# Performance work log

Measured on AMD Instinct MI355X. Metric: run time of the kernel, lower is better.

Reference implementation:

```python
import jax, jax.numpy as jnp
import numpy as np
from jax import lax

NMS_TH = 0.05
TOPK_P = 1000
NMS_IOU = 0.5
NUMDETS = 100
NMS_ITERS = 15
IM = 2048.0
SIZES = [256, 128, 64, 32, 16]
NUM_CLASS = 80


def _make_boxes(key, n):
    k1, k2, k3, k4 = jax.random.split(key, 4)
    cy = jax.random.uniform(k1, (n,)) * IM
    cx = jax.random.uniform(k2, (n,)) * IM
    h = jax.random.uniform(k3, (n,)) * 300.0 + 16.0
    w = jax.random.uniform(k4, (n,)) * 300.0 + 16.0
    # yxyx boxes
    return jnp.stack([cy - h / 2, cx - w / 2, cy + h / 2, cx + w / 2], axis=1)


def setup_inputs() -> dict:
    key = jax.random.key(0)
    inp = {}
    for s, sz in enumerate(SIZES):
        kc = jax.random.fold_in(key, 2 * s)
        kb = jax.random.fold_in(key, 2 * s + 1)
        n = sz * sz
        inp['cls%d' % s] = jax.random.normal(kc, (1, n, NUM_CLASS), jnp.float32) - 2.0
        inp['reg%d' % s] = _make_boxes(kb, n)[None]
    inp['locations'] = jnp.array([0.0, 0.0, IM - 1.0, IM - 1.0, 1024.0, 1024.0], jnp.float32)
    return inp


def _pairwise_iou(a, b):
    # a: (N,4) yxyx, b: (M,4) yxyx -> (N,M)
    area_a = jnp.clip(a[:, 2] - a[:, 0], 0) * jnp.clip(a[:, 3] - a[:, 1], 0)
    area_b = jnp.clip(b[:, 2] - b[:, 0], 0) * jnp.clip(b[:, 3] - b[:, 1], 0)
    iy1 = jnp.maximum(a[:, None, 0], b[None, :, 0])
    ix1 = jnp.maximum(a[:, None, 1], b[None, :, 1])
    iy2 = jnp.minimum(a[:, None, 2], b[None, :, 2])
    ix2 = jnp.minimum(a[:, None, 3], b[None, :, 3])
    inter = jnp.clip(iy2 - iy1, 0) * jnp.clip(ix2 - ix1, 0)
    union = area_a[:, None] + area_b[None, :] - inter
    return inter / jnp.maximum(union, 1e-9)


def _cluster_nms(boxes, scores, classes, valid, iou_th):
    order = jnp.argsort(-scores)
    b = boxes[order]
    s = scores[order]
    c = classes[order]
    v = valid[order]
    iou = jnp.triu(_pairwise_iou(b, b), k=1)  # (K,K)

    def body(B, _):
        max_a = B.max(axis=0)
        keep_col = (max_a <= iou_th).astype(B.dtype)[:, None]
        return iou * keep_col, None

    B, _ = lax.scan(body, iou, None, length=NMS_ITERS)
    keep = (B.max(axis=0) <= iou_th) & v
    return b, s, c, keep


def _per_level(cls_s, reg_s):
    p = jax.nn.sigmoid(cls_s[0])                 # (N, C)
    ps = p.max(axis=1)                           # (N,)
    pi = p.argmax(axis=1).astype(jnp.int32) + 1  # class index, 0 is background
    m = ps > NMS_TH
    ps_m = jnp.where(m, ps, -1.0)
    k = min(TOPK_P, ps_m.shape[0])
    top_s, top_idx = lax.top_k(ps_m, k)
    return top_s, pi[top_idx], reg_s[0][top_idx], m[top_idx]


def reference(cls0, cls1, cls2, cls3, cls4, reg0, reg1, reg2, reg3, reg4, locations):
    levels = [(cls0, reg0), (cls1, reg1), (cls2, reg2), (cls3, reg3), (cls4, reg4)]
    sc, cl, bx, vd = [], [], [], []
    for cls_s, reg_s in levels:
        s_, c_, b_, v_ = _per_level(cls_s, reg_s)
        sc.append(s_); cl.append(c_); bx.append(b_); vd.append(v_)
    scores = jnp.concatenate(sc)
    classes = jnp.concatenate(cl)
    boxes = jnp.concatenate(bx, axis=0)
    valid = jnp.concatenate(vd)
    scores = jnp.where(valid, scores, 0.0)

    vy1, vx1, vy2, vx2 = locations[0], locations[1], locations[2], locations[3]
    ori_h, ori_w = locations[4], locations[5]
    boxes = jnp.stack([
        jnp.maximum(boxes[:, 0], vy1), jnp.maximum(boxes[:, 1], vx1),
        jnp.minimum(boxes[:, 2], vy2), jnp.minimum(boxes[:, 3], vx2)], axis=1)

    b, s, c, keep = _cluster_nms(boxes, scores, classes, valid, NMS_IOU)
    s = jnp.where(keep, s, 0.0)
    top_s, sel = lax.top_k(s, NUMDETS)
    bbox = b[sel]
    cls_out = c[sel]

    # transfer boxes back to original-image coordinates
    sy = ori_h / jnp.maximum(vy2 - vy1, 1e-6)
    sx = ori_w / jnp.maximum(vx2 - vx1, 1e-6)
    bbox = jnp.stack([
        (bbox[:, 0] - vy1) * sy, (bbox[:, 1] - vx1) * sx,
        (bbox[:, 2] - vy1) * sy, (bbox[:, 3] - vx1) * sx], axis=1)
    return bbox, cls_out, top_s
```

## Files before the change

kernel.cpp:

```cpp
#include <hip/hip_runtime.h>
#include <math.h>


#define NANCH 87296
#define NF 4256
#define CAPD 128
#define NITER 16
#define BCAP 512
#define EC 8192
#define NBLK 341
#define BASE20 0xBD4CCu
#define NB20 9216
#define BPT 9

struct InPtrs {
    const float* cls[5];
    const float* reg[5];
    const float* loc;
};

constexpr size_t SZ_HIST  = 5ull * NB20 * 4;
constexpr size_t OFF_HIST = 0;
constexpr size_t OFF_CNT  = OFF_HIST + SZ_HIST;
constexpr size_t OFF_CTR  = OFF_CNT + (size_t)NF * 4;
constexpr size_t ZERO_SZ  = OFF_CTR + 128;
constexpr size_t OFF_SBITS = ((ZERO_SZ + 255) / 256) * 256;
constexpr size_t OFF_CLSV  = OFF_SBITS + (size_t)NANCH * 4;
constexpr size_t OFF_PAR   = OFF_CLSV + (size_t)NANCH * 4;
constexpr size_t OFF_INVB  = OFF_PAR + 128;
constexpr size_t OFF_INVO  = OFF_INVB + (size_t)NBLK * 4;
constexpr size_t OFF_FINK  = ((OFF_INVO + (size_t)NBLK * 4 + 255) / 256) * 256;
constexpr size_t OFF_BBUF  = OFF_FINK + (size_t)NF * 8;
constexpr size_t OFF_SBOX  = OFF_BBUF + 5ull * BCAP * 8;
constexpr size_t OFF_SSC   = OFF_SBOX + (size_t)NF * 16;
constexpr size_t OFF_SCV   = OFF_SSC + (size_t)NF * 4;
constexpr size_t OFF_SAR   = OFF_SCV + (size_t)NF * 4;
constexpr size_t OFF_NBR   = OFF_SAR + (size_t)NF * 4;

__device__ __forceinline__ void lvl_of(int a, int& lev, int& idx) {
    if (a < 65536)      { lev = 0; idx = a; }
    else if (a < 81920) { lev = 1; idx = a - 65536; }
    else if (a < 86016) { lev = 2; idx = a - 81920; }
    else if (a < 87040) { lev = 3; idx = a - 86016; }
    else                { lev = 4; idx = a - 87040; }
}

__device__ __forceinline__ unsigned int fkey(float f) {
    unsigned int u = __float_as_uint(f);
    return u ^ ((u & 0x80000000u) ? 0xFFFFFFFFu : 0x80000000u);
}
__device__ __forceinline__ float funkey(unsigned int k) {
    return __uint_as_float(k ^ ((k & 0x80000000u) ? 0x80000000u : 0xFFFFFFFFu));
}
__device__ __forceinline__ unsigned int bin20_addr(unsigned int v) {
    unsigned int owner = v / BPT;
    unsigned int i = v - owner * BPT;
    return (i << 10) | owner;
}
__device__ __forceinline__ unsigned int ald(const unsigned int* p) {
    return __hip_atomic_load((unsigned int*)p, __ATOMIC_RELAXED, __HIP_MEMORY_SCOPE_AGENT);
}
__device__ __forceinline__ void ast64(unsigned long long* p, unsigned long long v) {
    __hip_atomic_store(p, v, __ATOMIC_RELAXED, __HIP_MEMORY_SCOPE_AGENT);
}
__device__ __forceinline__ unsigned long long ald64(const unsigned long long* p) {
    return __hip_atomic_load((unsigned long long*)p, __ATOMIC_RELAXED, __HIP_MEMORY_SCOPE_AGENT);
}

__global__ __launch_bounds__(1024) void k1_score(InPtrs P, unsigned int* hist,
        unsigned int* sbits, unsigned int* clsv, unsigned int* invBlk) {
    int t = threadIdx.x;
    int a = blockIdx.x * 256 + (t >> 2);
    int k = t & 3;
    int lev, idx; lvl_of(a, lev, idx);
    const float4* row = (const float4*)(P.cls[lev] + (size_t)idx * 80);
    float4 v[5];
    #pragma unroll
    for (int q = 0; q < 5; ++q) v[q] = row[q * 4 + k];
    float best = -INFINITY; int bi = 0;
    #pragma unroll
    for (int q = 0; q < 5; ++q) {
        int c0 = q * 16 + k * 4;
        if (v[q].x > best) { best = v[q].x; bi = c0 + 0; }
        if (v[q].y > best) { best = v[q].y; bi = c0 + 1; }
        if (v[q].z > best) { best = v[q].z; bi = c0 + 2; }
        if (v[q].w > best) { best = v[q].w; bi = c0 + 3; }
    }
    #pragma unroll
    for (int m = 1; m < 4; m <<= 1) {
        float ob = __shfl_xor(best, m, 64);
        int  obi = __shfl_xor(bi, m, 64);
        if (ob > best || (ob == best && obi < bi)) { best = ob; bi = obi; }
    }
    bool lead = (k == 0);
    unsigned int valid = 0;
    if (lead) {
        float score = 1.0f / (1.0f + expf(-best));
        valid = (score > 0.05f) ? 1u : 0u;
        float psm = valid ? score : -1.0f;
        unsigned int sb = fkey(psm);
        sbits[a] = sb;
        clsv[a] = (unsigned int)(bi + 1) | (valid << 31);
        if (valid) {
            unsigned int bin = (sb >> 12) - BASE20;
            atomicAdd(&hist[(size_t)lev * NB20 + bin20_addr(bin)], 1u);
        }
    }
    __shared__ unsigned int wv[16];
    unsigned long long mv = __ballot(lead && valid);
    int lane = t & 63, w = t >> 6;
    if (lane == 0) wv[w] = (unsigned int)__popcll(mv);
    __syncthreads();
    if (t == 0) {
        unsigned int s = 0;
        #pragma unroll
        for (int i = 0; i < 16; ++i) s += wv[i];
        invBlk[blockIdx.x] = 256u - s;
    }
}

__global__ __launch_bounds__(1024) void k2_scan(const unsigned int* hist,
        const unsigned int* invBlk, unsigned int* params, unsigned int* invOff) {
    int t = threadIdx.x;
    if (blockIdx.x == 5) {
        __shared__ unsigned int sv[512];
        __shared__ unsigned int orig[512];
        if (t < 512) {
            unsigned int v = (t < NBLK) ? invBlk[t] : 0u;
            sv[t] = v; orig[t] = v;
        }
        __syncthreads();
        for (int off = 1; off < 512; off <<= 1) {
            unsigned int add = 0;
            if (t < 512 && t >= off) add = sv[t - off];
            __syncthreads();
            if (t < 512) sv[t] += add;
            __syncthreads();
        }
        if (t < NBLK) {
            int segStart = (t < 256) ? 0 : (t < 320) ? 256 : (t < 336) ? 320
                         : (t < 340) ? 336 : 340;
            invOff[t] = sv[t] - orig[t] - (segStart > 0 ? sv[segStart - 1] : 0u);
        }
        return;
    }
    int lev = blockIdx.x;
    unsigned int K = (lev == 4) ? 256u : 1000u;
    const unsigned int* h = hist + (size_t)lev * NB20;
    __shared__ unsigned int seg[1024];
    __shared__ unsigned int suf[1024];
    unsigned int hc[BPT];
    unsigned int s = 0;
    #pragma unroll
    for (int i = 0; i < BPT; ++i) { hc[i] = h[(i << 10) | t]; s += hc[i]; }
    seg[t] = s;
    suf[t] = s;
    __syncthreads();
    for (int off = 1; off < 1024; off <<= 1) {
        unsigned int v = suf[t];
        unsigned int add = (t + off < 1024) ? suf[t + off] : 0u;
        __syncthreads();
        suf[t] = v + add;
        __syncthreads();
    }
    unsigned int totValid = suf[0];
    if (totValid >= K) {
        unsigned int excl = suf[t] - seg[t];
        if (excl < K && excl + seg[t] >= K) {
            unsigned int cum = excl;
            for (int i = BPT - 1; i >= 0; --i) {
                unsigned int c = hc[i];
                if (cum + c >= K) {
                    params[lev] = (unsigned int)(t * BPT + i);
                    params[8 + lev] = K - cum;
                    params[16 + lev] = 0;
                    break;
                }
                cum += c;
            }
        }
    } else if (t == 0) {
        params[lev] = 0;
        params[8 + lev] = 0;
        params[16 + lev] = K - totValid;
    }
}

__global__ __launch_bounds__(256) void k3_compact(const unsigned int* sbits,
        const unsigned int* clsv, const unsigned int* params,
        const unsigned int* invOff, unsigned long long* finKeys,
        unsigned int* ctrs, unsigned long long* bBuf) {
    int blk = blockIdx.x;
    int t = threadIdx.x;
    int a = blk * 256 + t;
    int lev, idx; lvl_of(a, lev, idx);
    unsigned int sb = sbits[a];
    unsigned int cv = clsv[a];
    unsigned int bin = (sb >> 12) - BASE20;
    unsigned int Bs = params[lev];
    unsigned int rNeg = params[16 + lev];
    unsigned int valid = cv >> 31;
    int lane = t & 63, w = t >> 6;
    unsigned long long lt = (1ull << lane) - 1ull;
    __shared__ unsigned int wInv[4], wFin[4], wB[4];
    __shared__ unsigned int baseFin, baseB;
    unsigned long long mInv = __ballot(valid == 0u);
    if (lane == 0) wInv[w] = (unsigned int)__popcll(mInv);
    __syncthreads();
    unsigned int invRank = invOff[blk] + (unsigned int)__popcll(mInv & lt);
    for (int i = 0; i < w; ++i) invRank += wInv[i];
    bool isFin, isB;
    if (valid) {
        isFin = (bin > Bs);
        isB   = (bin == Bs);
    } else {
        isFin = (rNeg > 0) && (invRank < rNeg);
        isB   = false;
    }
    unsigned long long mFin = __ballot(isFin);
    unsigned long long mB   = __ballot(isB);
    if (lane == 0) { wFin[w] = (unsigned int)__popcll(mFin); wB[w] = (unsigned int)__popcll(mB); }
    __syncthreads();
    if (t == 0) {
        unsigned int tf = wFin[0] + wFin[1] + wFin[2] + wFin[3];
        unsigned int tb = wB[0] + wB[1] + wB[2] + wB[3];
        baseFin = tf ? atomicAdd(&ctrs[0], tf) : 0u;
        baseB   = tb ? atomicAdd(&ctrs[1 + lev], tb) : 0u;
    }
    __syncthreads();
    if (isFin || isB) {
        unsigned int composite = ((unsigned int)lev << 16) | (unsigned int)idx;
        unsigned int inv = (~composite) & 0x7FFFFu;
        unsigned int low = (inv << 13) | (valid << 7) | (cv & 0x7Fu);
        unsigned long long key = ((unsigned long long)sb << 32) | low;
        if (isFin) {
            unsigned int p = baseFin + (unsigned int)__popcll(mFin & lt);
            for (int i = 0; i < w; ++i) p += wFin[i];
            if (p < NF) finKeys[p] = key;
        } else {
            unsigned int p = baseB + (unsigned int)__popcll(mB & lt);
            for (int i = 0; i < w; ++i) p += wB[i];
            if (p < BCAP) ast64(&bBuf[(size_t)lev * BCAP + p], key);
        }
    }
    __shared__ unsigned int isLast;
    __shared__ unsigned long long kb[BCAP];
    __shared__ unsigned int posS;
    __syncthreads();
    if (t == 0) {
        asm volatile("s_waitcnt vmcnt(0)" ::: "memory");
        unsigned int r = __hip_atomic_fetch_add(&ctrs[8], 1u,
                             __ATOMIC_RELAXED, __HIP_MEMORY_SCOPE_AGENT);
        isLast = (r == (unsigned int)(NBLK - 1)) ? 1u : 0u;
    }
    __syncthreads();
    if (!isLast) return;
    unsigned int fc = ald(&ctrs[0]);
    if (fc > NF) fc = NF;
    if (t == 0) posS = fc;
    __syncthreads();
    for (int blev = 0; blev < 5; ++blev) {
        unsigned int bc = ald(&ctrs[1 + blev]);
        int n = (bc > BCAP) ? BCAP : (int)bc;
        int r = (int)params[8 + blev];
        if (r > n) r = n;
        if (r > 0) {
            for (int i = t; i < n; i += 256)
                kb[i] = ald64(&bBuf[(size_t)blev * BCAP + i]);
            __syncthreads();
            for (int i = t; i < n; i += 256) {
                unsigned long long my = kb[i];
                unsigned int c = 0;
                for (int j = 0; j < n; ++j) c += (kb[j] > my) ? 1u : 0u;
                if (c < (unsigned int)r) {
                    unsigned int p = atomicAdd(&posS, 1u);
                    if (p < NF) finKeys[p] = my;
                }
            }
            __syncthreads();
        }
    }
    for (int i = (int)posS + t; i < NF; i += 256)
        finKeys[i] = (unsigned long long)i;
}

__global__ __launch_bounds__(1024) void k5_rank(InPtrs P,
        const unsigned long long* finKeys,
        float4* sBox, float* sScore, unsigned int* sCV, float* sArea) {
    __shared__ __align__(16) unsigned long long keys[NF];
    __shared__ unsigned int rnk[64];
    int t = threadIdx.x;
    {
        const ulonglong2* src = (const ulonglong2*)finKeys;
        ulonglong2* dst = (ulonglong2*)keys;
        for (int i = t; i < NF / 2; i += 1024) dst[i] = src[i];
    }
    if (t < 64) rnk[t] = 0;
    __syncthreads();
    int lf = t & 63;
    int seg = t >> 6;
    int f = blockIdx.x * 64 + lf;
    unsigned long long my = (f < NF) ? keys[f] : 0ull;
    if (f < NF) {
        unsigned int c = 0;
        const ulonglong2* kp = (const ulonglong2*)keys + seg * 133;
        #pragma unroll 4
        for (int i = 0; i < 133; ++i) {
            ulonglong2 v = kp[i];
            c += (v.x > my) ? 1u : 0u;
            c += (v.y > my) ? 1u : 0u;
        }
        atomicAdd(&rnk[lf], c);
    }
    __syncthreads();
    if (seg == 0 && f < NF) {
        unsigned int r = rnk[lf];
        unsigned int sb  = (unsigned int)(my >> 32);
        unsigned int low = (unsigned int)my;
        unsigned int composite = (~(low >> 13)) & 0x7FFFFu;
        int lev = composite >> 16;
        int idx = composite & 0xFFFF;
        float4 b = ((const float4*)P.reg[lev])[idx];
        float vy1 = P.loc[0], vx1 = P.loc[1], vy2 = P.loc[2], vx2 = P.loc[3];
        float y1 = fmaxf(b.x, vy1), x1 = fmaxf(b.y, vx1);
        float y2 = fminf(b.z, vy2), x2 = fminf(b.w, vx2);
        float area = __fmul_rn(fmaxf(y2 - y1, 0.0f), fmaxf(x2 - x1, 0.0f));
        unsigned int valid = (low >> 7) & 1u;
        sBox[r] = make_float4(y1, x1, y2, x2);
        sScore[r] = valid ? funkey(sb) : 0.0f;
        sCV[r] = (low & 0x7Fu) | (valid << 31);
        sArea[r] = area;
    }
}

__global__ __launch_bounds__(256) void k6_adj(const float4* sBox,
        const float* sArea, unsigned int* cnt, unsigned short* nbr) {
    int L = blockIdx.x;
    float fr = sqrtf(8.0f * (float)L + 1.0f);
    int jt = (int)((fr - 1.0f) * 0.5f);
    while ((jt + 1) * (jt + 2) / 2 <= L) jt++;
    while (jt * (jt + 1) / 2 > L) jt--;
    int it = L - jt * (jt + 1) / 2;
    __shared__ float4 cb[64]; __shared__ float ca[64];
    __shared__ float4 rb[64]; __shared__ float ra[64];
    int t = threadIdx.x;
    if (t < 64) {
        int j = jt * 64 + t;
        if (j < NF) { cb[t] = sBox[j]; ca[t] = sArea[j]; }
        int i = it * 64 + t;
        if (i < NF) { rb[t] = sBox[i]; ra[t] = sArea[i]; }
    }
    __syncthreads();
    int lj = t & 63;
    int j = jt * 64 + lj;
    if (j >= NF) return;
    float4 B = cb[lj]; float ab = ca[lj];
    for (int li = (t >> 6); li < 64; li += 4) {
        int i = it * 64 + li;
        if (i >= j) continue;
        float4 A = rb[li]; float aa = ra[li];
        float iy1 = fmaxf(A.x, B.x), ix1 = fmaxf(A.y, B.y);
        float iy2 = fminf(A.z, B.z), ix2 = fminf(A.w, B.w);
        float ih = fmaxf(iy2 - iy1, 0.0f), iw = fmaxf(ix2 - ix1, 0.0f);
        float inter = __fmul_rn(ih, iw);
        float uni = __fsub_rn(__fadd_rn(aa, ab), inter);
        float iou = __fdiv_rn(inter, fmaxf(uni, 1e-9f));
        if (iou > 0.5f) {
            unsigned int p = atomicAdd(&cnt[j], 1u);
            if (p < CAPD) nbr[(size_t)j * CAPD + p] = (unsigned short)i;
        }
    }
}

__global__ __launch_bounds__(1024) void k7_nms(InPtrs P, const float4* sBox,
        const float* sScore, const unsigned int* sCV, const unsigned int* cnt,
        const unsigned short* nbr, float* out) {
    __shared__ unsigned int edges[EC];
    __shared__ __align__(4) unsigned char bufA[NF];
    __shared__ __align__(4) unsigned char bufB[NF];
    __shared__ unsigned int wsum[16];
    __shared__ float ploc[6];
    __shared__ unsigned int chg;
    int t = threadIdx.x;
    int lane = t & 63, wid = t >> 6;
    if (t < 6) ploc[t] = P.loc[t];
    const int CH = 5;
    unsigned int dq[CH];
    unsigned int s = 0;
    #pragma unroll
    for (int q = 0; q < CH; ++q) {
        int j = t * CH + q;
        unsigned int d = 0;
        if (j < NF) { d = cnt[j]; if (d > CAPD) d = CAPD; }
        dq[q] = d; s += d;
    }
    unsigned int sc = s;
    #pragma unroll
    for (int o = 1; o < 64; o <<= 1) {
        unsigned int n = __shfl_up(sc, o, 64);
        if (lane >= o) sc += n;
    }
    if (lane == 63) wsum[wid] = sc;
    if (t < 1064) ((unsigned int*)bufA)[t] = 0x01010101u;
    __syncthreads();
    unsigned int wbase = 0, tot = 0;
    #pragma unroll
    for (int i = 0; i < 16; ++i) {
        unsigned int v = wsum[i];
        if (i < wid) wbase += v;
        tot += v;
    }
    unsigned int E = tot;
    bool useLds = (E <= (unsigned int)EC);
    if (useLds) {
        unsigned int base = wbase + sc - s;
        #pragma unroll
        for (int q = 0; q < CH; ++q) {
            int j = t * CH + q;
            if (j < NF) {
                unsigned int d = dq[q];
                const unsigned short* nl = nbr + (size_t)j * CAPD;
                for (unsigned int e = 0; e < d; ++e)
                    edges[base + e] = ((unsigned int)nl[e] << 16) | (unsigned int)j;
                base += d;
            }
        }
    }
    __syncthreads();
    unsigned char* cur = bufA; unsigned char* nxt = bufB;
    for (int itr = 0; itr < NITER; ++itr) {
        if (t < 1064) ((unsigned int*)nxt)[t] = 0x01010101u;
        __syncthreads();
        if (useLds) {
            for (int e = t; e < (int)E; e += 1024) {
                unsigned int pk = edges[e];
                if (cur[pk >> 16]) nxt[pk & 0xFFFFu] = 0;
            }
        } else {
            for (int j = t; j < NF; j += 1024) {
                unsigned int d = cnt[j]; if (d > CAPD) d = CAPD;
                const unsigned short* nl = nbr + (size_t)j * CAPD;
                unsigned int hit = 0;
                for (unsigned int e = 0; e < d; ++e)
                    hit |= (unsigned int)cur[nl[e]];
                if (hit) nxt[j] = 0;
            }
        }
        __syncthreads();
        if (t < 1064 &&
            ((unsigned int*)nxt)[t] != ((unsigned int*)cur)[t]) chg = 1;
        __syncthreads();
        unsigned int done = (chg == 0u);
        unsigned char* tm = cur; cur = nxt; nxt = tm;
        __syncthreads();
        if (t == 0) chg = 0;
        if (done) break;
    }
    int base = t * CH;
    unsigned char kf[CH];
    unsigned int sum = 0;
    #pragma unroll
    for (int q = 0; q < CH; ++q) {
        int j = base + q;
        unsigned char v = 0;
        if (j < NF) v = cur[j] & (unsigned char)(sCV[j] >> 31);
        kf[q] = v; sum += v;
    }
    unsigned int sc2 = sum;
    #pragma unroll
    for (int o = 1; o < 64; o <<= 1) {
        unsigned int n = __shfl_up(sc2, o, 64);
        if (lane >= o) sc2 += n;
    }
    if (lane == 63) wsum[wid] = sc2;
    __syncthreads();
    unsigned int wbase2 = 0, keptTot = 0;
    #pragma unroll
    for (int i = 0; i < 16; ++i) {
        unsigned int v = wsum[i];
        if (i < wid) wbase2 += v;
        keptTot += v;
    }
    unsigned int run = wbase2 + sc2 - sum;
    float vy1 = ploc[0], vx1 = ploc[1], vy2 = ploc[2], vx2 = ploc[3];
    float sy = ploc[4] / fmaxf(vy2 - vy1, 1e-6f);
    float sx = ploc[5] / fmaxf(vx2 - vx1, 1e-6f);
    #pragma unroll
    for (int q = 0; q < CH; ++q) {
        int j = base + q;
        if (j >= NF) break;
        unsigned int slot = 0xFFFFFFFFu;
        float scv = 0.0f;
        if (kf[q]) {
            if (run < 100u) { slot = run; scv = sScore[j]; }
            run++;
        } else if (keptTot < 100u) {
            unsigned int nk = (unsigned int)j - run;
            unsigned int s2 = keptTot + nk;
            if (s2 < 100u) { slot = s2; scv = 0.0f; }
        }
        if (slot < 100u) {
            float4 b = sBox[j];
            out[slot * 4 + 0] = (b.x - vy1) * sy;
            out[slot * 4 + 1] = (b.y - vx1) * sx;
            out[slot * 4 + 2] = (b.z - vy1) * sy;
            out[slot * 4 + 3] = (b.w - vx1) * sx;
            out[400 + slot] = (float)(sCV[j] & 0x7Fu);
            out[500 + slot] = scv;
        }
    }
}

extern "C" void kernel_launch(void* const* d_in, const int* in_sizes, int n_in,
                              void* d_out, int out_size, void* d_ws, size_t ws_size,
                              hipStream_t stream) {
    (void)n_in; (void)out_size; (void)ws_size;
    InPtrs P;
    bool inter = (in_sizes[1] == 65536 * 4);
    for (int s = 0; s < 5; ++s) {
        P.cls[s] = (const float*)d_in[inter ? 2 * s : s];
        P.reg[s] = (const float*)d_in[inter ? 2 * s + 1 : 5 + s];
    }
    P.loc = (const float*)d_in[10];

    char* w = (char*)d_ws;
    unsigned int* hist   = (unsigned int*)(w + OFF_HIST);
    unsigned int* cnt    = (unsigned int*)(w + OFF_CNT);
    unsigned int* ctrs   = (unsigned int*)(w + OFF_CTR);
    unsigned int* sbits  = (unsigned int*)(w + OFF_SBITS);
    unsigned int* clsv   = (unsigned int*)(w + OFF_CLSV);
    unsigned int* params = (unsigned int*)(w + OFF_PAR);
    unsigned int* invBlk = (unsigned int*)(w + OFF_INVB);
    unsigned int* invOff = (unsigned int*)(w + OFF_INVO);
    unsigned long long* finKeys = (unsigned long long*)(w + OFF_FINK);
    unsigned long long* bBuf    = (unsigned long long*)(w + OFF_BBUF);
    float4* sBox  = (float4*)(w + OFF_SBOX);
    float* sScore = (float*)(w + OFF_SSC);
    unsigned int* sCV = (unsigned int*)(w + OFF_SCV);
    float* sArea  = (float*)(w + OFF_SAR);
    unsigned short* nbr = (unsigned short*)(w + OFF_NBR);

    hipMemsetAsync(d_ws, 0, ZERO_SZ, stream);
    k1_score<<<NBLK, 1024, 0, stream>>>(P, hist, sbits, clsv, invBlk);
    k2_scan<<<6, 1024, 0, stream>>>(hist, invBlk, params, invOff);
    k3_compact<<<NBLK, 256, 0, stream>>>(sbits, clsv, params, invOff, finKeys, ctrs, bBuf);
    k5_rank<<<67, 1024, 0, stream>>>(P, finKeys, sBox, sScore, sCV, sArea);
    k6_adj<<<2278, 256, 0, stream>>>(sBox, sArea, cnt, nbr);
    k7_nms<<<1, 1024, 0, stream>>>(P, sBox, sScore, sCV, cnt, nbr, (float*)d_out);
}
```

Measured before the change: 173.0 us.

## Fuse scan, compact and rank kernels; merge adjacency and NMS via last-block pattern

Reduces the pipeline from six launches to three. Each compact block now recomputes the per-level histogram threshold scan and its own invalid-prefix offset redundantly. The last-arriving block merges the tie buckets, and the final 67 arriving blocks spin-wait on a flag, then do the global rank scatter. The adjacency tiles and the cluster NMS are also fused: the last tile block runs the iterative suppression with 256 threads instead of 1024. This removes launch gaps and kernel boundaries, but adds redundant histogram reads, a spin-wait that depends on co-resident blocks, and a single-block NMS with fewer threads and a wider int neighbor array.

```diff
diff --git a/kernel.cpp b/kernel.cpp
--- a/kernel.cpp
+++ b/kernel.cpp
@@ -12,6 +12,8 @@
 #define BASE20 0xBD4CCu
 #define NB20 9216
 #define BPT 9
+#define NTILE 2278
+#define NRANK 67
 
 struct InPtrs {
     const float* cls[5];
@@ -28,8 +30,7 @@
 constexpr size_t OFF_CLSV  = OFF_SBITS + (size_t)NANCH * 4;
 constexpr size_t OFF_PAR   = OFF_CLSV + (size_t)NANCH * 4;
 constexpr size_t OFF_INVB  = OFF_PAR + 128;
-constexpr size_t OFF_INVO  = OFF_INVB + (size_t)NBLK * 4;
-constexpr size_t OFF_FINK  = ((OFF_INVO + (size_t)NBLK * 4 + 255) / 256) * 256;
+constexpr size_t OFF_FINK  = ((OFF_INVB + (size_t)NBLK * 4 + 255) / 256) * 256;
 constexpr size_t OFF_BBUF  = OFF_FINK + (size_t)NF * 8;
 constexpr size_t OFF_SBOX  = OFF_BBUF + 5ull * BCAP * 8;
 constexpr size_t OFF_SSC   = OFF_SBOX + (size_t)NF * 16;
@@ -59,6 +60,9 @@
 }
 __device__ __forceinline__ unsigned int ald(const unsigned int* p) {
     return __hip_atomic_load((unsigned int*)p, __ATOMIC_RELAXED, __HIP_MEMORY_SCOPE_AGENT);
+}
+__device__ __forceinline__ void ast(unsigned int* p, unsigned int v) {
+    __hip_atomic_store(p, v, __ATOMIC_RELAXED, __HIP_MEMORY_SCOPE_AGENT);
 }
 __device__ __forceinline__ void ast64(unsigned long long* p, unsigned long long v) {
     __hip_atomic_store(p, v, __ATOMIC_RELAXED, __HIP_MEMORY_SCOPE_AGENT);
@@ -119,107 +123,103 @@
     }
 }
 
-__global__ __launch_bounds__(1024) void k2_scan(const unsigned int* hist,
-        const unsigned int* invBlk, unsigned int* params, unsigned int* invOff) {
+__global__ __launch_bounds__(256) void k3_all(InPtrs P, const unsigned int* hist,
+        const unsigned int* sbits, const unsigned int* clsv,
+        const unsigned int* invBlk, unsigned int* params, unsigned int* ctrs,
+        unsigned long long* finKeys, unsigned long long* bBuf,
+        float4* sBox, float* sScore, unsigned int* sCV, float* sArea) {
+    int blk = blockIdx.x;
     int t = threadIdx.x;
-    if (blockIdx.x == 5) {
-        __shared__ unsigned int sv[512];
-        __shared__ unsigned int orig[512];
-        if (t < 512) {
-            unsigned int v = (t < NBLK) ? invBlk[t] : 0u;
-            sv[t] = v; orig[t] = v;
-        }
-        __syncthreads();
-        for (int off = 1; off < 512; off <<= 1) {
-            unsigned int add = 0;
-            if (t < 512 && t >= off) add = sv[t - off];
-            __syncthreads();
-            if (t < 512) sv[t] += add;
-            __syncthreads();
-        }
-        if (t < NBLK) {
-            int segStart = (t < 256) ? 0 : (t < 320) ? 256 : (t < 336) ? 320
-                         : (t < 340) ? 336 : 340;
-            invOff[t] = sv[t] - orig[t] - (segStart > 0 ? sv[segStart - 1] : 0u);
-        }
-        return;
-    }
-    int lev = blockIdx.x;
+    int lane = t & 63, wid = t >> 6;
+
+    int lev, segStart;
+    if (blk < 256)      { lev = 0; segStart = 0; }
+    else if (blk < 320) { lev = 1; segStart = 256; }
+    else if (blk < 336) { lev = 2; segStart = 320; }
+    else if (blk < 340) { lev = 3; segStart = 336; }
+    else                { lev = 4; segStart = 340; }
     unsigned int K = (lev == 4) ? 256u : 1000u;
     const unsigned int* h = hist + (size_t)lev * NB20;
-    __shared__ unsigned int seg[1024];
-    __shared__ unsigned int suf[1024];
-    unsigned int hc[BPT];
-    unsigned int s = 0;
-    #pragma unroll
-    for (int i = 0; i < BPT; ++i) { hc[i] = h[(i << 10) | t]; s += hc[i]; }
-    seg[t] = s;
-    suf[t] = s;
+
+    __shared__ union {
+        struct { unsigned int osum[1024]; } pre;
+        struct { unsigned long long kb[BCAP]; } tl;
+        struct { unsigned long long keys[NF]; unsigned int rnk[64]; } rk;
+    } u;
+    __shared__ unsigned int red[4];
+    __shared__ unsigned int sBs, sR, sRneg;
+    __shared__ unsigned int wInv[4], wFin[4], wB[4];
+    __shared__ unsigned int baseFin, baseB, myRank, posS;
+
+    unsigned int s4[4];
+    #pragma unroll
+    for (int c = 0; c < 4; ++c) {
+        int ow = t + (c << 8);
+        unsigned int s = 0;
+        #pragma unroll
+        for (int i = 0; i < BPT; ++i) s += h[(i << 10) | ow];
+        s4[c] = s; u.pre.osum[ow] = s;
+    }
     __syncthreads();
     for (int off = 1; off < 1024; off <<= 1) {
-        unsigned int v = suf[t];
-        unsigned int add = (t + off < 1024) ? suf[t + off] : 0u;
-        __syncthreads();
-        suf[t] = v + add;
-        __syncthreads();
-    }
-    unsigned int totValid = suf[0];
+        unsigned int v[4], a2[4];
+        #pragma unroll
+        for (int c = 0; c < 4; ++c) {
+            int idx = t + (c << 8);
+            v[c] = u.pre.osum[idx];
+            a2[c] = (idx + off < 1024) ? u.pre.osum[idx + off] : 0u;
+        }
+        __syncthreads();
+        #pragma unroll
+        for (int c = 0; c < 4; ++c) { int idx = t + (c << 8); u.pre.osum[idx] = v[c] + a2[c]; }
+        __syncthreads();
+    }
+    unsigned int totValid = u.pre.osum[0];
     if (totValid >= K) {
-        unsigned int excl = suf[t] - seg[t];
-        if (excl < K && excl + seg[t] >= K) {
-            unsigned int cum = excl;
-            for (int i = BPT - 1; i >= 0; --i) {
-                unsigned int c = hc[i];
-                if (cum + c >= K) {
-                    params[lev] = (unsigned int)(t * BPT + i);
-                    params[8 + lev] = K - cum;
-                    params[16 + lev] = 0;
-                    break;
+        #pragma unroll
+        for (int c = 0; c < 4; ++c) {
+            int ow = t + (c << 8);
+            unsigned int osuf = u.pre.osum[ow];
+            unsigned int excl = osuf - s4[c];
+            if (excl < K && osuf >= K) {
+                unsigned int cum = excl;
+                for (int i = BPT - 1; i >= 0; --i) {
+                    unsigned int cc = h[(i << 10) | ow];
+                    if (cum + cc >= K) { sBs = (unsigned int)(ow * BPT + i);
+                                         sR = K - cum; sRneg = 0; break; }
+                    cum += cc;
                 }
-                cum += c;
             }
         }
-    } else if (t == 0) {
-        params[lev] = 0;
-        params[8 + lev] = 0;
-        params[16 + lev] = K - totValid;
-    }
-}
-
-__global__ __launch_bounds__(256) void k3_compact(const unsigned int* sbits,
-        const unsigned int* clsv, const unsigned int* params,
-        const unsigned int* invOff, unsigned long long* finKeys,
-        unsigned int* ctrs, unsigned long long* bBuf) {
-    int blk = blockIdx.x;
-    int t = threadIdx.x;
+    } else if (t == 0) { sBs = 0; sR = 0; sRneg = K - totValid; }
+    unsigned int lsum = 0;
+    for (int i = segStart + t; i < blk; i += 256) lsum += invBlk[i];
+    #pragma unroll
+    for (int m = 1; m < 64; m <<= 1) lsum += __shfl_xor(lsum, m, 64);
+    if (lane == 0) red[wid] = lsum;
+    __syncthreads();
+    unsigned int invOffBlk = red[0] + red[1] + red[2] + red[3];
+    unsigned int Bs = sBs, rNeg = sRneg;
+    if (blk == segStart && t == 0) ast(&params[8 + lev], sR);
+
     int a = blk * 256 + t;
-    int lev, idx; lvl_of(a, lev, idx);
     unsigned int sb = sbits[a];
     unsigned int cv = clsv[a];
     unsigned int bin = (sb >> 12) - BASE20;
-    unsigned int Bs = params[lev];
-    unsigned int rNeg = params[16 + lev];
     unsigned int valid = cv >> 31;
-    int lane = t & 63, w = t >> 6;
     unsigned long long lt = (1ull << lane) - 1ull;
-    __shared__ unsigned int wInv[4], wFin[4], wB[4];
-    __shared__ unsigned int baseFin, baseB;
     unsigned long long mInv = __ballot(valid == 0u);
-    if (lane == 0) wInv[w] = (unsigned int)__popcll(mInv);
-    __syncthreads();
-    unsigned int invRank = invOff[blk] + (unsigned int)__popcll(mInv & lt);
-    for (int i = 0; i < w; ++i) invRank += wInv[i];
+    if (lane == 0) wInv[wid] = (unsigned int)__popcll(mInv);
+    __syncthreads();
+    unsigned int invRank = invOffBlk + (unsigned int)__popcll(mInv & lt);
+    for (int i = 0; i < wid; ++i) invRank += wInv[i];
     bool isFin, isB;
-    if (valid) {
-        isFin = (bin > Bs);
-        isB   = (bin == Bs);
-    } else {
-        isFin = (rNeg > 0) && (invRank < rNeg);
-        isB   = false;
-    }
+    if (valid) { isFin = (bin > Bs); isB = (bin == Bs); }
+    else       { isFin = (rNeg > 0) && (invRank < rNeg); isB = false; }
     unsigned long long mFin = __ballot(isFin);
     unsigned long long mB   = __ballot(isB);
-    if (lane == 0) { wFin[w] = (unsigned int)__popcll(mFin); wB[w] = (unsigned int)__popcll(mB); }
+    if (lane == 0) { wFin[wid] = (unsigned int)__popcll(mFin);
+                     wB[wid]   = (unsigned int)__popcll(mB); }
     __syncthreads();
     if (t == 0) {
         unsigned int tf = wFin[0] + wFin[1] + wFin[2] + wFin[3];
@@ -229,169 +229,179 @@
     }
     __syncthreads();
     if (isFin || isB) {
-        unsigned int composite = ((unsigned int)lev << 16) | (unsigned int)idx;
+        int lidx = a - segStart * 256;
+        unsigned int composite = ((unsigned int)lev << 16) | (unsigned int)lidx;
         unsigned int inv = (~composite) & 0x7FFFFu;
         unsigned int low = (inv << 13) | (valid << 7) | (cv & 0x7Fu);
         unsigned long long key = ((unsigned long long)sb << 32) | low;
         if (isFin) {
             unsigned int p = baseFin + (unsigned int)__popcll(mFin & lt);
-            for (int i = 0; i < w; ++i) p += wFin[i];
-            if (p < NF) finKeys[p] = key;
+            for (int i = 0; i < wid; ++i) p += wFin[i];
+            if (p < NF) ast64(&finKeys[p], key);
         } else {
             unsigned int p = baseB + (unsigned int)__popcll(mB & lt);
-            for (int i = 0; i < w; ++i) p += wB[i];
+            for (int i = 0; i < wid; ++i) p += wB[i];
             if (p < BCAP) ast64(&bBuf[(size_t)lev * BCAP + p], key);
         }
     }
-    __shared__ unsigned int isLast;
-    __shared__ unsigned long long kb[BCAP];
-    __shared__ unsigned int posS;
+
     __syncthreads();
     if (t == 0) {
         asm volatile("s_waitcnt vmcnt(0)" ::: "memory");
-        unsigned int r = __hip_atomic_fetch_add(&ctrs[8], 1u,
-                             __ATOMIC_RELAXED, __HIP_MEMORY_SCOPE_AGENT);
-        isLast = (r == (unsigned int)(NBLK - 1)) ? 1u : 0u;
-    }
-    __syncthreads();
-    if (!isLast) return;
-    unsigned int fc = ald(&ctrs[0]);
-    if (fc > NF) fc = NF;
-    if (t == 0) posS = fc;
-    __syncthreads();
-    for (int blev = 0; blev < 5; ++blev) {
-        unsigned int bc = ald(&ctrs[1 + blev]);
-        int n = (bc > BCAP) ? BCAP : (int)bc;
-        int r = (int)params[8 + blev];
-        if (r > n) r = n;
-        if (r > 0) {
-            for (int i = t; i < n; i += 256)
-                kb[i] = ald64(&bBuf[(size_t)blev * BCAP + i]);
-            __syncthreads();
-            for (int i = t; i < n; i += 256) {
-                unsigned long long my = kb[i];
-                unsigned int c = 0;
-                for (int j = 0; j < n; ++j) c += (kb[j] > my) ? 1u : 0u;
-                if (c < (unsigned int)r) {
-                    unsigned int p = atomicAdd(&posS, 1u);
-                    if (p < NF) finKeys[p] = my;
+        myRank = __hip_atomic_fetch_add(&ctrs[8], 1u,
+                     __ATOMIC_RELAXED, __HIP_MEMORY_SCOPE_AGENT);
+    }
+    __syncthreads();
+    unsigned int rk_ = myRank;
+    if (rk_ < (unsigned int)(NBLK - 1 - NRANK)) return;
+
+    if (rk_ == (unsigned int)(NBLK - 1)) {
+        unsigned int fc = ald(&ctrs[0]);
+        if (fc > NF) fc = NF;
+        if (t == 0) posS = fc;
+        __syncthreads();
+        for (int blev = 0; blev < 5; ++blev) {
+            unsigned int bc = ald(&ctrs[1 + blev]);
+            int n = (bc > BCAP) ? BCAP : (int)bc;
+            int r = (int)ald(&params[8 + blev]);
+            if (r > n) r = n;
+            if (r > 0) {
+                for (int i = t; i < n; i += 256)
+                    u.tl.kb[i] = ald64(&bBuf[(size_t)blev * BCAP + i]);
+                __syncthreads();
+                for (int i = t; i < n; i += 256) {
+                    unsigned long long my = u.tl.kb[i];
+                    unsigned int c = 0;
+                    for (int j = 0; j < n; ++j) c += (u.tl.kb[j] > my) ? 1u : 0u;
+                    if (c < (unsigned int)r) {
+                        unsigned int p = atomicAdd(&posS, 1u);
+                        if (p < NF) ast64(&finKeys[p], my);
+                    }
                 }
+                __syncthreads();
             }
-            __syncthreads();
-        }
-    }
-    for (int i = (int)posS + t; i < NF; i += 256)
-        finKeys[i] = (unsigned long long)i;
-}
-
-__global__ __launch_bounds__(1024) void k5_rank(InPtrs P,
-        const unsigned long long* finKeys,
-        float4* sBox, float* sScore, unsigned int* sCV, float* sArea) {
-    __shared__ __align__(16) unsigned long long keys[NF];
-    __shared__ unsigned int rnk[64];
-    int t = threadIdx.x;
-    {
-        const ulonglong2* src = (const ulonglong2*)finKeys;
-        ulonglong2* dst = (ulonglong2*)keys;
-        for (int i = t; i < NF / 2; i += 1024) dst[i] = src[i];
-    }
-    if (t < 64) rnk[t] = 0;
+        }
+        __syncthreads();
+        for (int i = (int)posS + t; i < NF; i += 256)
+            ast64(&finKeys[i], (unsigned long long)i);
+        __syncthreads();
+        if (t == 0) {
+            asm volatile("s_waitcnt vmcnt(0)" ::: "memory");
+            ast(&ctrs[10], 1u);
+        }
+        return;
+    }
+
+    if (t == 0) {
+        int g = 0;
+        while (ald(&ctrs[10]) == 0u && g < 200000) { __builtin_amdgcn_s_sleep(8); ++g; }
+    }
+    __syncthreads();
+    int rb = (int)rk_ - (NBLK - 1 - NRANK);
+    for (int i = t; i < NF; i += 256) u.rk.keys[i] = ald64(&finKeys[i]);
+    if (t < 64) u.rk.rnk[t] = 0;
     __syncthreads();
     int lf = t & 63;
     int seg = t >> 6;
-    int f = blockIdx.x * 64 + lf;
-    unsigned long long my = (f < NF) ? keys[f] : 0ull;
+    int f = rb * 64 + lf;
+    unsigned long long my = (f < NF) ? u.rk.keys[f] : 0ull;
     if (f < NF) {
         unsigned int c = 0;
-        const ulonglong2* kp = (const ulonglong2*)keys + seg * 133;
-        #pragma unroll 4
-        for (int i = 0; i < 133; ++i) {
-            ulonglong2 v = kp[i];
-            c += (v.x > my) ? 1u : 0u;
-            c += (v.y > my) ? 1u : 0u;
-        }
-        atomicAdd(&rnk[lf], c);
+        const unsigned long long* kp = u.rk.keys + seg * 1064;
+        #pragma unroll 8
+        for (int i = 0; i < 1064; ++i) c += (kp[i] > my) ? 1u : 0u;
+        atomicAdd(&u.rk.rnk[lf], c);
     }
     __syncthreads();
     if (seg == 0 && f < NF) {
-        unsigned int r = rnk[lf];
-        unsigned int sb  = (unsigned int)(my >> 32);
+        unsigned int r = u.rk.rnk[lf];
+        unsigned int sbv = (unsigned int)(my >> 32);
         unsigned int low = (unsigned int)my;
         unsigned int composite = (~(low >> 13)) & 0x7FFFFu;
-        int lev = composite >> 16;
+        int lev2 = composite >> 16;
         int idx = composite & 0xFFFF;
-        float4 b = ((const float4*)P.reg[lev])[idx];
+        float4 b = ((const float4*)P.reg[lev2])[idx];
         float vy1 = P.loc[0], vx1 = P.loc[1], vy2 = P.loc[2], vx2 = P.loc[3];
         float y1 = fmaxf(b.x, vy1), x1 = fmaxf(b.y, vx1);
         float y2 = fminf(b.z, vy2), x2 = fminf(b.w, vx2);
         float area = __fmul_rn(fmaxf(y2 - y1, 0.0f), fmaxf(x2 - x1, 0.0f));
-        unsigned int valid = (low >> 7) & 1u;
+        unsigned int valid2 = (low >> 7) & 1u;
         sBox[r] = make_float4(y1, x1, y2, x2);
-        sScore[r] = valid ? funkey(sb) : 0.0f;
-        sCV[r] = (low & 0x7Fu) | (valid << 31);
+        sScore[r] = valid2 ? funkey(sbv) : 0.0f;
+        sCV[r] = (low & 0x7Fu) | (valid2 << 31);
         sArea[r] = area;
     }
 }
 
-__global__ __launch_bounds__(256) void k6_adj(const float4* sBox,
-        const float* sArea, unsigned int* cnt, unsigned short* nbr) {
-    int L = blockIdx.x;
-    float fr = sqrtf(8.0f * (float)L + 1.0f);
-    int jt = (int)((fr - 1.0f) * 0.5f);
-    while ((jt + 1) * (jt + 2) / 2 <= L) jt++;
-    while (jt * (jt + 1) / 2 > L) jt--;
-    int it = L - jt * (jt + 1) / 2;
+__global__ __launch_bounds__(256) void k6_nms(InPtrs P, const float4* sBox,
+        const float* sArea, const float* sScore, const unsigned int* sCV,
+        unsigned int* cnt, unsigned int* nbr, unsigned int* ctrs,
+        float* __restrict__ out) {
     __shared__ float4 cb[64]; __shared__ float ca[64];
-    __shared__ float4 rb[64]; __shared__ float ra[64];
-    int t = threadIdx.x;
-    if (t < 64) {
-        int j = jt * 64 + t;
-        if (j < NF) { cb[t] = sBox[j]; ca[t] = sArea[j]; }
-        int i = it * 64 + t;
-        if (i < NF) { rb[t] = sBox[i]; ra[t] = sArea[i]; }
-    }
-    __syncthreads();
-    int lj = t & 63;
-    int j = jt * 64 + lj;
-    if (j >= NF) return;
-    float4 B = cb[lj]; float ab = ca[lj];
-    for (int li = (t >> 6); li < 64; li += 4) {
-        int i = it * 64 + li;
-        if (i >= j) continue;
-        float4 A = rb[li]; float aa = ra[li];
-        float iy1 = fmaxf(A.x, B.x), ix1 = fmaxf(A.y, B.y);
-        float iy2 = fminf(A.z, B.z), ix2 = fminf(A.w, B.w);
-        float ih = fmaxf(iy2 - iy1, 0.0f), iw = fmaxf(ix2 - ix1, 0.0f);
-        float inter = __fmul_rn(ih, iw);
-        float uni = __fsub_rn(__fadd_rn(aa, ab), inter);
-        float iou = __fdiv_rn(inter, fmaxf(uni, 1e-9f));
-        if (iou > 0.5f) {
-            unsigned int p = atomicAdd(&cnt[j], 1u);
-            if (p < CAPD) nbr[(size_t)j * CAPD + p] = (unsigned short)i;
-        }
-    }
-}
-
-__global__ __launch_bounds__(1024) void k7_nms(InPtrs P, const float4* sBox,
-        const float* sScore, const unsigned int* sCV, const unsigned int* cnt,
-        const unsigned short* nbr, float* out) {
+    __shared__ float4 rbx[64]; __shared__ float ra[64];
     __shared__ unsigned int edges[EC];
     __shared__ __align__(4) unsigned char bufA[NF];
     __shared__ __align__(4) unsigned char bufB[NF];
-    __shared__ unsigned int wsum[16];
+    __shared__ unsigned int wsum[4];
     __shared__ float ploc[6];
-    __shared__ unsigned int chg;
+    __shared__ unsigned int chg, rk2;
     int t = threadIdx.x;
     int lane = t & 63, wid = t >> 6;
+
+    {
+        int L = blockIdx.x;
+        float fr = sqrtf(8.0f * (float)L + 1.0f);
+        int jt = (int)((fr - 1.0f) * 0.5f);
+        while ((jt + 1) * (jt + 2) / 2 <= L) jt++;
+        while (jt * (jt + 1) / 2 > L) jt--;
+        int it = L - jt * (jt + 1) / 2;
+        if (t < 64) {
+            int j = jt * 64 + t;
+            if (j < NF) { cb[t] = sBox[j]; ca[t] = sArea[j]; }
+            int i = it * 64 + t;
+            if (i < NF) { rbx[t] = sBox[i]; ra[t] = sArea[i]; }
+        }
+        __syncthreads();
+        int lj = t & 63;
+        int j = jt * 64 + lj;
+        if (j < NF) {
+            float4 B = cb[lj]; float ab = ca[lj];
+            for (int li = (t >> 6); li < 64; li += 4) {
+                int i = it * 64 + li;
+                if (i >= j) continue;
+                float4 A = rbx[li]; float aa = ra[li];
+                float iy1 = fmaxf(A.x, B.x), ix1 = fmaxf(A.y, B.y);
+                float iy2 = fminf(A.z, B.z), ix2 = fminf(A.w, B.w);
+                float ih = fmaxf(iy2 - iy1, 0.0f), iw = fmaxf(ix2 - ix1, 0.0f);
+                float inter = __fmul_rn(ih, iw);
+                float uni = __fsub_rn(__fadd_rn(aa, ab), inter);
+                float iou = __fdiv_rn(inter, fmaxf(uni, 1e-9f));
+                if (iou > 0.5f) {
+                    unsigned int p = atomicAdd(&cnt[j], 1u);
+                    if (p < CAPD) ast(&nbr[(size_t)j * CAPD + p], (unsigned int)i);
+                }
+            }
+        }
+    }
+    __syncthreads();
+    if (t == 0) {
+        asm volatile("s_waitcnt vmcnt(0)" ::: "memory");
+        rk2 = __hip_atomic_fetch_add(&ctrs[9], 1u,
+                  __ATOMIC_RELAXED, __HIP_MEMORY_SCOPE_AGENT);
+    }
+    __syncthreads();
+    if (rk2 != (unsigned int)(NTILE - 1)) return;
+
+    const int CH = 17;
     if (t < 6) ploc[t] = P.loc[t];
-    const int CH = 5;
+    if (t == 0) chg = 0;
     unsigned int dq[CH];
     unsigned int s = 0;
     #pragma unroll
     for (int q = 0; q < CH; ++q) {
         int j = t * CH + q;
         unsigned int d = 0;
-        if (j < NF) { d = cnt[j]; if (d > CAPD) d = CAPD; }
+        if (j < NF) { d = ald(&cnt[j]); if (d > CAPD) d = CAPD; }
         dq[q] = d; s += d;
     }
     unsigned int sc = s;
@@ -401,11 +411,11 @@
         if (lane >= o) sc += n;
     }
     if (lane == 63) wsum[wid] = sc;
-    if (t < 1064) ((unsigned int*)bufA)[t] = 0x01010101u;
+    for (int i = t; i < 1064; i += 256) ((unsigned int*)bufA)[i] = 0x01010101u;
     __syncthreads();
     unsigned int wbase = 0, tot = 0;
     #pragma unroll
-    for (int i = 0; i < 16; ++i) {
+    for (int i = 0; i < 4; ++i) {
         unsigned int v = wsum[i];
         if (i < wid) wbase += v;
         tot += v;
@@ -419,9 +429,9 @@
             int j = t * CH + q;
             if (j < NF) {
                 unsigned int d = dq[q];
-                const unsigned short* nl = nbr + (size_t)j * CAPD;
+                const unsigned int* nl = nbr + (size_t)j * CAPD;
                 for (unsigned int e = 0; e < d; ++e)
-                    edges[base + e] = ((unsigned int)nl[e] << 16) | (unsigned int)j;
+                    edges[base + e] = (ald(&nl[e]) << 16) | (unsigned int)j;
                 base += d;
             }
         }
@@ -429,26 +439,26 @@
     __syncthreads();
     unsigned char* cur = bufA; unsigned char* nxt = bufB;
     for (int itr = 0; itr < NITER; ++itr) {
-        if (t < 1064) ((unsigned int*)nxt)[t] = 0x01010101u;
+        for (int i = t; i < 1064; i += 256) ((unsigned int*)nxt)[i] = 0x01010101u;
         __syncthreads();
         if (useLds) {
-            for (int e = t; e < (int)E; e += 1024) {
+            for (int e = t; e < (int)E; e += 256) {
                 unsigned int pk = edges[e];
                 if (cur[pk >> 16]) nxt[pk & 0xFFFFu] = 0;
             }
         } else {
-            for (int j = t; j < NF; j += 1024) {
-                unsigned int d = cnt[j]; if (d > CAPD) d = CAPD;
-                const unsigned short* nl = nbr + (size_t)j * CAPD;
+            for (int j = t; j < NF; j += 256) {
+                unsigned int d = ald(&cnt[j]); if (d > CAPD) d = CAPD;
+                const unsigned int* nl = nbr + (size_t)j * CAPD;
                 unsigned int hit = 0;
                 for (unsigned int e = 0; e < d; ++e)
-                    hit |= (unsigned int)cur[nl[e]];
+                    hit |= (unsigned int)cur[ald(&nl[e])];
                 if (hit) nxt[j] = 0;
             }
         }
         __syncthreads();
-        if (t < 1064 &&
-            ((unsigned int*)nxt)[t] != ((unsigned int*)cur)[t]) chg = 1;
+        for (int i = t; i < 1064; i += 256)
+            if (((unsigned int*)nxt)[i] != ((unsigned int*)cur)[i]) chg = 1;
         __syncthreads();
         unsigned int done = (chg == 0u);
         unsigned char* tm = cur; cur = nxt; nxt = tm;
@@ -456,12 +466,12 @@
         if (t == 0) chg = 0;
         if (done) break;
     }
-    int base = t * CH;
+    int base2 = t * CH;
     unsigned char kf[CH];
     unsigned int sum = 0;
     #pragma unroll
     for (int q = 0; q < CH; ++q) {
-        int j = base + q;
+        int j = base2 + q;
         unsigned char v = 0;
         if (j < NF) v = cur[j] & (unsigned char)(sCV[j] >> 31);
         kf[q] = v; sum += v;
@@ -476,7 +486,7 @@
     __syncthreads();
     unsigned int wbase2 = 0, keptTot = 0;
     #pragma unroll
-    for (int i = 0; i < 16; ++i) {
+    for (int i = 0; i < 4; ++i) {
         unsigned int v = wsum[i];
         if (i < wid) wbase2 += v;
         keptTot += v;
@@ -487,7 +497,7 @@
     float sx = ploc[5] / fmaxf(vx2 - vx1, 1e-6f);
     #pragma unroll
     for (int q = 0; q < CH; ++q) {
-        int j = base + q;
+        int j = base2 + q;
         if (j >= NF) break;
         unsigned int slot = 0xFFFFFFFFu;
         float scv = 0.0f;
@@ -531,20 +541,18 @@
     unsigned int* clsv   = (unsigned int*)(w + OFF_CLSV);
     unsigned int* params = (unsigned int*)(w + OFF_PAR);
     unsigned int* invBlk = (unsigned int*)(w + OFF_INVB);
-    unsigned int* invOff = (unsigned int*)(w + OFF_INVO);
     unsigned long long* finKeys = (unsigned long long*)(w + OFF_FINK);
     unsigned long long* bBuf    = (unsigned long long*)(w + OFF_BBUF);
     float4* sBox  = (float4*)(w + OFF_SBOX);
     float* sScore = (float*)(w + OFF_SSC);
     unsigned int* sCV = (unsigned int*)(w + OFF_SCV);
     float* sArea  = (float*)(w + OFF_SAR);
-    unsigned short* nbr = (unsigned short*)(w + OFF_NBR);
+    unsigned int* nbr = (unsigned int*)(w + OFF_NBR);
 
     hipMemsetAsync(d_ws, 0, ZERO_SZ, stream);
     k1_score<<<NBLK, 1024, 0, stream>>>(P, hist, sbits, clsv, invBlk);
-    k2_scan<<<6, 1024, 0, stream>>>(hist, invBlk, params, invOff);
-    k3_compact<<<NBLK, 256, 0, stream>>>(sbits, clsv, params, invOff, finKeys, ctrs, bBuf);
-    k5_rank<<<67, 1024, 0, stream>>>(P, finKeys, sBox, sScore, sCV, sArea);
-    k6_adj<<<2278, 256, 0, stream>>>(sBox, sArea, cnt, nbr);
-    k7_nms<<<1, 1024, 0, stream>>>(P, sBox, sScore, sCV, cnt, nbr, (float*)d_out);
-}
+    k3_all<<<NBLK, 256, 0, stream>>>(P, hist, sbits, clsv, invBlk, params, ctrs,
+                                     finKeys, bBuf, sBox, sScore, sCV, sArea);
+    k6_nms<<<NTILE, 256, 0, stream>>>(P, sBox, sArea, sScore, sCV, cnt, nbr,
+                                      ctrs, (float*)d_out);
+}
```

Result: slower. 245.2 us (+41.7%).
